# Kernel tuning notes

Hardware: AMD Instinct MI355X
Metric: run time of the kernel (lower is better)

The kernel has to match this reference:

```python
import jax, jax.numpy as jnp
import numpy as np

B, N, G, T, D = 32, 512, 64, 16, 256
E, M = 500000, 1024
NEG = jnp.float32(-1e10)


def setup_inputs() -> dict:
    key = jax.random.key(0)
    ks = jax.random.split(key, 8)
    scope_token_reprs = jax.random.normal(ks[0], (B, N, T, D), dtype=jnp.float32)
    goal_token_reprs = jax.random.normal(ks[1], (B, G, T, D), dtype=jnp.float32)
    W = jax.random.normal(ks[2], (1, D, D), dtype=jnp.float32) / np.sqrt(D)
    bias = jax.random.normal(ks[3], (1,), dtype=jnp.float32)
    src = jax.random.randint(ks[4], (E,), 0, B * N)
    tgt = jax.random.randint(ks[5], (E,), 0, B * G)
    edge_index = jnp.stack([src, tgt], axis=0)
    lm_mask_idx = jax.random.randint(ks[6], (M,), 0, B * N * T)
    batch_pts = lm_mask_idx // (N * T)  # consistent: each masked token belongs to its own batch element
    tree_mask = jax.random.uniform(ks[7], (B, N)) < 0.7
    return {
        'scope_token_reprs': scope_token_reprs,
        'goal_token_reprs': goal_token_reprs,
        'W': W,
        'bias': bias,
        'edge_index': edge_index,
        'lm_mask_idx': lm_mask_idx,
        'batch_pts': batch_pts,
        'tree_mask': tree_mask,
    }


def reference(scope_token_reprs, goal_token_reprs, W, bias, edge_index, lm_mask_idx, batch_pts, tree_mask):
    dim = scope_token_reprs.shape[-1]
    # --- predict_lemmas: edge gather + bilinear scoring ---
    scope_type = scope_token_reprs[:, :, 0].reshape(-1, dim)  # [B*N, D]
    goal_type = goal_token_reprs[:, :, 0].reshape(-1, dim)    # [B*G, D]
    sources = scope_type[edge_index[0]]                        # [E, D]
    targets = goal_type[edge_index[1]]                         # [E, D]
    lemma_preds = jnp.einsum('ed,df,ef->e', sources, W[0], targets) + bias[0]  # [E]
    # --- predict_masks: masked-token dot against candidate type reprs ---
    mask_reprs = scope_token_reprs.reshape(-1, dim)[lm_mask_idx]  # [M, D]
    type_reprs = scope_token_reprs[:, :, 0]                        # [B, N, D]
    candidates = type_reprs[batch_pts]                             # [M, N, D]
    candidate_mask = tree_mask[batch_pts]                          # [M, N]
    lm_preds = jnp.einsum('md,mnd->mn', mask_reprs, candidates)    # [M, N]
    lm_preds = jnp.where(candidate_mask, lm_preds, NEG)
    return lemma_preds, lm_preds
```

## Files before the change

### kernel.cpp

```cpp
#include <hip/hip_runtime.h>

#define B_   32
#define N_   512
#define G_   64
#define T_   16
#define D_   256
#define E_   500000
#define M_   1024
#define S_   (B_ * N_)
#define TT_  2048
#define TD_  (T_ * D_)
#define NEG_ (-10000000000.0f)

#define WS_WT    0
#define WS_WGB   262144
#define WS_SCB   2097152
#define WS_FLAG  10485760
#define WS_P     16777216

typedef short  short8 __attribute__((ext_vector_type(8)));
typedef float  f32x4  __attribute__((ext_vector_type(4)));

__device__ __forceinline__ unsigned short f2bf(float x) {
  union { float f; unsigned int u; } v; v.f = x;
  const unsigned int r = (v.u + 0x7fffu + ((v.u >> 16) & 1u)) >> 16;
  return (unsigned short)r;
}

__global__ __launch_bounds__(256) void detect_mask_dtype(
    const unsigned char* __restrict__ tm, int* __restrict__ flag) {
  __shared__ int sA, sB;
  if (threadIdx.x == 0) { sA = 0; sB = 0; }
  __syncthreads();
  int a = 0, b3 = 0;
  for (int i = threadIdx.x; i < B_ * N_; i += 256) {
    const int r = i & 3;
    const unsigned char v = tm[i];
    if (r == 1) a |= v;
    else if (r == 3) b3 |= v;
  }
  if (a)  atomicOr(&sA, 1);
  if (b3) atomicOr(&sB, 1);
  __syncthreads();
  if (threadIdx.x == 0) flag[0] = sA ? 1 : (sB ? 2 : 0);
}

__global__ __launch_bounds__(256) void transpose_w(
    const float* __restrict__ W, float* __restrict__ Wt) {
  __shared__ float tile[32][33];
  const int bi = blockIdx.x >> 3;
  const int bj = blockIdx.x & 7;
  const int tx = threadIdx.x & 31;
  const int ty = threadIdx.x >> 5;
#pragma unroll
  for (int r = 0; r < 4; r++)
    tile[ty + r * 8][tx] = W[(size_t)(bi * 32 + ty + r * 8) * D_ + bj * 32 + tx];
  __syncthreads();
#pragma unroll
  for (int r = 0; r < 4; r++)
    Wt[(size_t)(bj * 32 + ty + r * 8) * D_ + bi * 32 + tx] =
        tile[tx][ty + r * 8];
}

__global__ __launch_bounds__(256) void wg_gemm(
    const float* __restrict__ goal, const float* __restrict__ Wt,
    unsigned short* __restrict__ Wgb) {
  __shared__ float g[8][256];
  const int j0 = blockIdx.x * 8;
  const int d  = threadIdx.x;
  {
    const int lane = threadIdx.x & 63;
    const int r0   = threadIdx.x >> 6;
#pragma unroll
    for (int rr = 0; rr < 2; rr++) {
      const int row = rr * 4 + r0;
      const float4 v = *reinterpret_cast<const float4*>(
          goal + (size_t)(j0 + row) * TD_ + lane * 4);
      float* dst = &g[row][lane * 4];
      dst[0] = v.x; dst[1] = v.y; dst[2] = v.z; dst[3] = v.w;
    }
  }
  __syncthreads();
  float acc[8];
#pragma unroll
  for (int jj = 0; jj < 8; jj++) acc[jj] = 0.f;
#pragma unroll 4
  for (int f = 0; f < D_; f++) {
    const float w = Wt[(size_t)f * D_ + d];
#pragma unroll
    for (int jj = 0; jj < 8; jj++) acc[jj] = fmaf(g[jj][f], w, acc[jj]);
  }
#pragma unroll
  for (int jj = 0; jj < 8; jj++)
    Wgb[(size_t)(j0 + jj) * D_ + d] = f2bf(acc[jj]);
}

__global__ __launch_bounds__(256) void cast_scope(
    const float* __restrict__ scope, unsigned short* __restrict__ scb) {
  const int q   = blockIdx.x * 256 + threadIdx.x;
  const int row = q >> 6;
  const int c4  = q & 63;
  const float4 v =
      *reinterpret_cast<const float4*>(scope + (size_t)row * TD_ + c4 * 4);
  ushort4 o;
  o.x = f2bf(v.x); o.y = f2bf(v.y); o.z = f2bf(v.z); o.w = f2bf(v.w);
  *reinterpret_cast<ushort4*>(&scb[(size_t)row * D_ + c4 * 4]) = o;
}

#define BM 128
#define BN 128
#define BK 64
#define LDT 80

__global__ __launch_bounds__(256) void gemm_p(
    const unsigned short* __restrict__ scb,
    const unsigned short* __restrict__ wgb, float* __restrict__ P) {
  __shared__ unsigned short As[BM][LDT];
  __shared__ unsigned short Bs[BN][LDT];
  const int sB   = blockIdx.x >> 4;
  const int tB   = blockIdx.x & 15;
  const int tid  = threadIdx.x;
  const int lane = tid & 63;
  const int w    = tid >> 6;
  const int wr   = (w >> 1) * 64;
  const int wc   = (w & 1) * 64;
  const int lr   = lane & 15;
  const int lq   = lane >> 4;

  f32x4 acc[4][4];
#pragma unroll
  for (int mi = 0; mi < 4; mi++)
#pragma unroll
    for (int ni = 0; ni < 4; ni++)
      acc[mi][ni] = (f32x4){0.f, 0.f, 0.f, 0.f};

  const int r0 = tid >> 3;
  const int kg = tid & 7;

  for (int ks = 0; ks < D_ / BK; ks++) {
    __syncthreads();
#pragma unroll
    for (int rr = 0; rr < 4; rr++) {
      const int row = r0 + rr * 32;
      *reinterpret_cast<uint4*>(&As[row][kg * 8]) =
          *reinterpret_cast<const uint4*>(
              &scb[(size_t)(sB * BM + row) * D_ + ks * BK + kg * 8]);
      *reinterpret_cast<uint4*>(&Bs[row][kg * 8]) =
          *reinterpret_cast<const uint4*>(
              &wgb[(size_t)(tB * BN + row) * D_ + ks * BK + kg * 8]);
    }
    __syncthreads();
#pragma unroll
    for (int s16 = 0; s16 < 2; s16++) {
      const int koff = s16 * 32 + lq * 8;
      short8 aF[4], bF[4];
#pragma unroll
      for (int mi = 0; mi < 4; mi++)
        aF[mi] = *reinterpret_cast<const short8*>(&As[wr + mi * 16 + lr][koff]);
#pragma unroll
      for (int ni = 0; ni < 4; ni++)
        bF[ni] = *reinterpret_cast<const short8*>(&Bs[wc + ni * 16 + lr][koff]);
#pragma unroll
      for (int mi = 0; mi < 4; mi++)
#pragma unroll
        for (int ni = 0; ni < 4; ni++)
          acc[mi][ni] = __builtin_amdgcn_mfma_f32_16x16x32_bf16(
              aF[mi], bF[ni], acc[mi][ni], 0, 0, 0);
    }
  }

#pragma unroll
  for (int mi = 0; mi < 4; mi++) {
#pragma unroll
    for (int ni = 0; ni < 4; ni++) {
      const int colg = tB * BN + wc + ni * 16 + lr;
#pragma unroll
      for (int r = 0; r < 4; r++) {
        const int rowg = sB * BM + wr + mi * 16 + lq * 4 + r;
        P[(size_t)rowg * TT_ + colg] = acc[mi][ni][r];
      }
    }
  }
}

__global__ __launch_bounds__(256) void gather_edges(
    const float* __restrict__ P, const int* __restrict__ edges,
    const float* __restrict__ bias, float* __restrict__ out) {
  const int e = blockIdx.x * 256 + threadIdx.x;
  if (e >= E_) return;
  const int s = edges[e];
  const int t = edges[E_ + e];
  out[e] = P[(size_t)s * TT_ + t] + bias[0];
}

__global__ __launch_bounds__(256) void lm_kernel(
    const float* __restrict__ scope, const int* __restrict__ lm_idx,
    const int* __restrict__ batch_pts, const void* __restrict__ tree_mask,
    const int* __restrict__ flag_p, float* __restrict__ out) {
  __shared__ float cand[32][260];
  __shared__ unsigned char tmask[32];
  __shared__ int mlist[M_];
  __shared__ int mcnt;
  const int b  = blockIdx.x >> 4;
  const int n0 = (blockIdx.x & 15) * 32;
  const int t  = threadIdx.x;

  if (t == 0) mcnt = 0;
  {
    const int lane = t & 63;
    const int r0   = t >> 6;
#pragma unroll
    for (int rr = 0; rr < 8; rr++) {
      const int row = rr * 4 + r0;
      const float4 v = *reinterpret_cast<const float4*>(
          scope + (size_t)(b * N_ + n0 + row) * TD_ + lane * 4);
      float* dst = &cand[row][lane * 4];
      dst[0] = v.x; dst[1] = v.y; dst[2] = v.z; dst[3] = v.w;
    }
  }
  const int flag = flag_p[0];
  if (t < 32) {
    const int n = b * N_ + n0 + t;
    int v;
    if (flag == 1)      v = ((const unsigned char*)tree_mask)[n] != 0;
    else if (flag == 2) v = ((const float*)tree_mask)[n] != 0.0f;
    else                v = ((const int*)tree_mask)[n] != 0;
    tmask[t] = (unsigned char)v;
  }
  __syncthreads();

#pragma unroll
  for (int c = 0; c < M_ / 256; c++) {
    const int m = c * 256 + t;
    if (batch_pts[m] == b) {
      const int p = atomicAdd(&mcnt, 1);
      mlist[p] = m;
    }
  }
  __syncthreads();
  const int cnt = mcnt;

  const int nl = t >> 3;
  const int kg = t & 7;
  for (int k = 0; k < cnt; k++) {
    const int m = mlist[k];
    const float4* q =
        reinterpret_cast<const float4*>(scope + (size_t)lm_idx[m] * D_);
    float acc = 0.f;
#pragma unroll
    for (int i = 0; i < 8; i++) {
      const int f4 = kg * 8 + i;
      const float4 qv = q[f4];
      const float* cp = &cand[nl][f4 * 4];
      acc += qv.x * cp[0] + qv.y * cp[1] + qv.z * cp[2] + qv.w * cp[3];
    }
    acc += __shfl_xor(acc, 1);
    acc += __shfl_xor(acc, 2);
    acc += __shfl_xor(acc, 4);
    if (kg == 0)
      out[(size_t)m * N_ + (n0 + nl)] = tmask[nl] ? acc : NEG_;
  }
}

extern "C" void kernel_launch(void* const* d_in, const int* in_sizes, int n_in,
                              void* d_out, int out_size, void* d_ws,
                              size_t ws_size, hipStream_t stream) {
  const float* scope = (const float*)d_in[0];
  const float* goal  = (const float*)d_in[1];
  const float* W     = (const float*)d_in[2];
  const float* bias  = (const float*)d_in[3];
  const int*   edges = (const int*)d_in[4];
  const int*   lmidx = (const int*)d_in[5];
  const int*   bpts  = (const int*)d_in[6];
  const void*  tmask = d_in[7];

  float* out = (float*)d_out;
  char*  ws  = (char*)d_ws;
  float*          Wt   = (float*)(ws + WS_WT);
  unsigned short* Wgb  = (unsigned short*)(ws + WS_WGB);
  unsigned short* scb  = (unsigned short*)(ws + WS_SCB);
  int*            flag = (int*)(ws + WS_FLAG);
  float*          P    = (float*)(ws + WS_P);

  detect_mask_dtype<<<1, 256, 0, stream>>>((const unsigned char*)tmask, flag);
  transpose_w<<<64, 256, 0, stream>>>(W, Wt);
  wg_gemm<<<TT_ / 8, 256, 0, stream>>>(goal, Wt, Wgb);
  cast_scope<<<(S_ * 64) / 256, 256, 0, stream>>>(scope, scb);
  gemm_p<<<(S_ / BM) * (TT_ / BN), 256, 0, stream>>>(scb, Wgb, P);
  gather_edges<<<(E_ + 255) / 256, 256, 0, stream>>>(P, edges, bias, out);
  lm_kernel<<<B_ * 16, 256, 0, stream>>>(scope, lmidx, bpts, tmask, flag,
                                         out + E_);
}
```

Before: 483.8 us.

## Replace dense all-pairs score GEMM with per-edge gathered dot products

Instead of computing the full 16384x2048 score matrix P with an MFMA GEMM and then gathering 500k entries, each edge now loads its bf16 scope row and its precomputed W·goal row, and a 16-lane group computes the 256-wide dot product with shuffle reductions. This removes about 17 GFLOP of dense matmul and a 128 MB fp32 write plus random reads. The cost is about 1 KB of random gathered reads per edge, served mostly from cache since the source tables are small (8 MB and 1 MB).

```diff
diff --git a/kernel.cpp b/kernel.cpp
--- a/kernel.cpp
+++ b/kernel.cpp
@@ -16,15 +16,19 @@
 #define WS_WGB   262144
 #define WS_SCB   2097152
 #define WS_FLAG  10485760
-#define WS_P     16777216
 
 typedef short  short8 __attribute__((ext_vector_type(8)));
-typedef float  f32x4  __attribute__((ext_vector_type(4)));
 
 __device__ __forceinline__ unsigned short f2bf(float x) {
   union { float f; unsigned int u; } v; v.f = x;
   const unsigned int r = (v.u + 0x7fffu + ((v.u >> 16) & 1u)) >> 16;
   return (unsigned short)r;
+}
+
+__device__ __forceinline__ float bf2f(unsigned short u) {
+  union { unsigned int u; float f; } v;
+  v.u = ((unsigned int)u) << 16;
+  return v.f;
 }
 
 __global__ __launch_bounds__(256) void detect_mask_dtype(
@@ -107,90 +111,32 @@
   *reinterpret_cast<ushort4*>(&scb[(size_t)row * D_ + c4 * 4]) = o;
 }
 
-#define BM 128
-#define BN 128
-#define BK 64
-#define LDT 80
-
-__global__ __launch_bounds__(256) void gemm_p(
+__global__ __launch_bounds__(256) void edge_dot(
     const unsigned short* __restrict__ scb,
-    const unsigned short* __restrict__ wgb, float* __restrict__ P) {
-  __shared__ unsigned short As[BM][LDT];
-  __shared__ unsigned short Bs[BN][LDT];
-  const int sB   = blockIdx.x >> 4;
-  const int tB   = blockIdx.x & 15;
-  const int tid  = threadIdx.x;
-  const int lane = tid & 63;
-  const int w    = tid >> 6;
-  const int wr   = (w >> 1) * 64;
-  const int wc   = (w & 1) * 64;
-  const int lr   = lane & 15;
-  const int lq   = lane >> 4;
-
-  f32x4 acc[4][4];
-#pragma unroll
-  for (int mi = 0; mi < 4; mi++)
-#pragma unroll
-    for (int ni = 0; ni < 4; ni++)
-      acc[mi][ni] = (f32x4){0.f, 0.f, 0.f, 0.f};
-
-  const int r0 = tid >> 3;
-  const int kg = tid & 7;
-
-  for (int ks = 0; ks < D_ / BK; ks++) {
-    __syncthreads();
-#pragma unroll
-    for (int rr = 0; rr < 4; rr++) {
-      const int row = r0 + rr * 32;
-      *reinterpret_cast<uint4*>(&As[row][kg * 8]) =
-          *reinterpret_cast<const uint4*>(
-              &scb[(size_t)(sB * BM + row) * D_ + ks * BK + kg * 8]);
-      *reinterpret_cast<uint4*>(&Bs[row][kg * 8]) =
-          *reinterpret_cast<const uint4*>(
-              &wgb[(size_t)(tB * BN + row) * D_ + ks * BK + kg * 8]);
-    }
-    __syncthreads();
-#pragma unroll
-    for (int s16 = 0; s16 < 2; s16++) {
-      const int koff = s16 * 32 + lq * 8;
-      short8 aF[4], bF[4];
-#pragma unroll
-      for (int mi = 0; mi < 4; mi++)
-        aF[mi] = *reinterpret_cast<const short8*>(&As[wr + mi * 16 + lr][koff]);
-#pragma unroll
-      for (int ni = 0; ni < 4; ni++)
-        bF[ni] = *reinterpret_cast<const short8*>(&Bs[wc + ni * 16 + lr][koff]);
-#pragma unroll
-      for (int mi = 0; mi < 4; mi++)
-#pragma unroll
-        for (int ni = 0; ni < 4; ni++)
-          acc[mi][ni] = __builtin_amdgcn_mfma_f32_16x16x32_bf16(
-              aF[mi], bF[ni], acc[mi][ni], 0, 0, 0);
-    }
-  }
-
-#pragma unroll
-  for (int mi = 0; mi < 4; mi++) {
-#pragma unroll
-    for (int ni = 0; ni < 4; ni++) {
-      const int colg = tB * BN + wc + ni * 16 + lr;
-#pragma unroll
-      for (int r = 0; r < 4; r++) {
-        const int rowg = sB * BM + wr + mi * 16 + lq * 4 + r;
-        P[(size_t)rowg * TT_ + colg] = acc[mi][ni][r];
-      }
-    }
-  }
-}
-
-__global__ __launch_bounds__(256) void gather_edges(
-    const float* __restrict__ P, const int* __restrict__ edges,
-    const float* __restrict__ bias, float* __restrict__ out) {
-  const int e = blockIdx.x * 256 + threadIdx.x;
-  if (e >= E_) return;
+    const unsigned short* __restrict__ wgb,
+    const int* __restrict__ edges, const float* __restrict__ bias,
+    float* __restrict__ out) {
+  const int tid = threadIdx.x;
+  const int grp = tid >> 4;
+  const int l   = tid & 15;
+  const int e   = blockIdx.x * 16 + grp;
   const int s = edges[e];
   const int t = edges[E_ + e];
-  out[e] = P[(size_t)s * TT_ + t] + bias[0];
+  const short8 a0 = *reinterpret_cast<const short8*>(&scb[(size_t)s * D_ + l * 8]);
+  const short8 a1 = *reinterpret_cast<const short8*>(&scb[(size_t)s * D_ + 128 + l * 8]);
+  const short8 b0 = *reinterpret_cast<const short8*>(&wgb[(size_t)t * D_ + l * 8]);
+  const short8 b1 = *reinterpret_cast<const short8*>(&wgb[(size_t)t * D_ + 128 + l * 8]);
+  float acc = 0.f;
+#pragma unroll
+  for (int i = 0; i < 8; i++) {
+    acc = fmaf(bf2f((unsigned short)a0[i]), bf2f((unsigned short)b0[i]), acc);
+    acc = fmaf(bf2f((unsigned short)a1[i]), bf2f((unsigned short)b1[i]), acc);
+  }
+  acc += __shfl_xor(acc, 1);
+  acc += __shfl_xor(acc, 2);
+  acc += __shfl_xor(acc, 4);
+  acc += __shfl_xor(acc, 8);
+  if (l == 0) out[e] = acc + bias[0];
 }
 
 __global__ __launch_bounds__(256) void lm_kernel(
@@ -280,14 +226,12 @@
   unsigned short* Wgb  = (unsigned short*)(ws + WS_WGB);
   unsigned short* scb  = (unsigned short*)(ws + WS_SCB);
   int*            flag = (int*)(ws + WS_FLAG);
-  float*          P    = (float*)(ws + WS_P);
 
   detect_mask_dtype<<<1, 256, 0, stream>>>((const unsigned char*)tmask, flag);
   transpose_w<<<64, 256, 0, stream>>>(W, Wt);
   wg_gemm<<<TT_ / 8, 256, 0, stream>>>(goal, Wt, Wgb);
   cast_scope<<<(S_ * 64) / 256, 256, 0, stream>>>(scope, scb);
-  gemm_p<<<(S_ / BM) * (TT_ / BN), 256, 0, stream>>>(scb, Wgb, P);
-  gather_edges<<<(E_ + 255) / 256, 256, 0, stream>>>(P, edges, bias, out);
+  edge_dot<<<E_ / 16, 256, 0, stream>>>(scb, Wgb, edges, bias, out);
   lm_kernel<<<B_ * 16, 256, 0, stream>>>(scope, lmidx, bpts, tmask, flag,
                                          out + E_);
 }
```

Result: faster. 466.0 us (-3.7%).
